# Optimization experiments

Measured on AMD Instinct MI355X. Metric: run time of the kernel, lower is better.

Reference implementation:

```python
import jax, jax.numpy as jnp
import numpy as np

N, E, F_IN, H, L = 100000, 1600000, 256, 128, 4
ALPHA, THETA, EPS = 0.1, 0.5, 1e-5


def setup_inputs() -> dict:
    key = jax.random.key(0)
    ks = jax.random.split(key, 6)
    x = jax.random.normal(ks[0], (N, F_IN), dtype=jnp.float32)
    edge_index = jax.random.randint(ks[1], (2, E), 0, N, dtype=jnp.int32)
    lin0_w = jax.random.normal(ks[2], (F_IN, H), dtype=jnp.float32) / np.sqrt(F_IN)
    lin0_b = jnp.zeros((H,), dtype=jnp.float32)
    conv_w = jax.random.normal(ks[3], (L, H, H), dtype=jnp.float32) / np.sqrt(H)
    bn_gamma = jnp.ones((L - 1, H), dtype=jnp.float32)
    bn_beta = jnp.zeros((L - 1, H), dtype=jnp.float32)
    return {"x": x, "edge_index": edge_index, "lin0_w": lin0_w, "lin0_b": lin0_b,
            "conv_w": conv_w, "bn_gamma": bn_gamma, "bn_beta": bn_beta}


def reference(x, edge_index, lin0_w, lin0_b, conv_w, bn_gamma, bn_beta):
    n = x.shape[0]
    loops = jnp.arange(n, dtype=edge_index.dtype)
    row = jnp.concatenate([edge_index[0], loops])  # source
    col = jnp.concatenate([edge_index[1], loops])  # target
    # GCN symmetric normalization with self-loops: D^{-1/2}(A+I)D^{-1/2}
    deg = jax.ops.segment_sum(jnp.ones_like(col, dtype=x.dtype), col, num_segments=n)
    dinv = jnp.where(deg > 0, jax.lax.rsqrt(deg), 0.0)
    norm = (dinv[row] * dinv[col])[:, None]  # [E+N, 1]

    def prop(h):  # sparse aggregation: out[c] += norm * h[r]
        return jax.ops.segment_sum(h[row] * norm, col, num_segments=n)

    # GCNConv input layer
    z = prop(x @ lin0_w) + lin0_b
    x0 = z
    for i in range(L):
        h = prop(z)
        beta = float(np.log(THETA / (i + 1) + 1.0))
        s = (1.0 - ALPHA) * h + ALPHA * x0          # identity mapping to initial features
        z = (1.0 - beta) * s + beta * (s @ conv_w[i])  # shared_weights GCN2Conv
        if i < L - 1:
            mu = jnp.mean(z, axis=0)
            var = jnp.mean((z - mu) ** 2, axis=0)
            z = (z - mu) * jax.lax.rsqrt(var + EPS) * bn_gamma[i] + bn_beta[i]
            z = jax.nn.relu(z)
    return z
```

## Files before the change

### kernel.cpp

```cpp
#include <hip/hip_runtime.h>
#include <hip/hip_bf16.h>
#include <math.h>

#define H 128
#define EPS_BN 1e-5f
#define RSTATS 16

typedef __attribute__((ext_vector_type(8))) short short8;
typedef __attribute__((ext_vector_type(4))) float f32x4;

__device__ __forceinline__ float bf2f(ushort u){
  union { float f; uint v; } x; x.v = ((uint)u) << 16; return x.f;
}
__device__ __forceinline__ ushort f2bf(float f){
  union { float f; uint v; } x; x.f = f;
  uint v = x.v;
  uint r = v + 0x7fff + ((v >> 16) & 1);
  return (ushort)(r >> 16);
}

__device__ __forceinline__ void acc8(float* a, uint4 v, float wt){
  a[0] += wt*bf2f((ushort)(v.x & 0xffff)); a[1] += wt*bf2f((ushort)(v.x >> 16));
  a[2] += wt*bf2f((ushort)(v.y & 0xffff)); a[3] += wt*bf2f((ushort)(v.y >> 16));
  a[4] += wt*bf2f((ushort)(v.z & 0xffff)); a[5] += wt*bf2f((ushort)(v.z >> 16));
  a[6] += wt*bf2f((ushort)(v.w & 0xffff)); a[7] += wt*bf2f((ushort)(v.w >> 16));
}


__global__ void k_count(const int* __restrict__ col, int E, int* __restrict__ cnt){
  int i = blockIdx.x*blockDim.x + threadIdx.x;
  if (i < E) atomicAdd(&cnt[col[i]], 1);
}

__global__ void k_dinv(const int* __restrict__ cnt, float* __restrict__ dinv, int n){
  int i = blockIdx.x*blockDim.x + threadIdx.x;
  if (i < n) dinv[i] = rsqrtf((float)cnt[i] + 1.0f);
}

__global__ void k_scan1(const int* __restrict__ cnt, int* __restrict__ off,
                        int* __restrict__ bsum, int n){
  __shared__ int s[1024];
  int t = threadIdx.x;
  int i = blockIdx.x*1024 + t;
  int v = (i < n) ? cnt[i] : 0;
  s[t] = v; __syncthreads();
  for (int d = 1; d < 1024; d <<= 1){
    int x = (t >= d) ? s[t-d] : 0;
    __syncthreads();
    s[t] += x;
    __syncthreads();
  }
  if (i < n) off[i] = s[t] - v;
  if (t == 1023) bsum[blockIdx.x] = s[1023];
}

__global__ void k_scan2(int* bsum, int nb){
  int l = threadIdx.x;
  int carry = 0;
  for (int b0 = 0; b0 < nb; b0 += 64){
    int i = b0 + l;
    int orig = (i < nb) ? bsum[i] : 0;
    int v = orig;
    #pragma unroll
    for (int d = 1; d < 64; d <<= 1){
      int x = __shfl_up(v, d);
      if (l >= d) v += x;
    }
    if (i < nb) bsum[i] = carry + v - orig;
    carry += __shfl(v, 63);
  }
}

__global__ void k_scan3(int* __restrict__ off, int* __restrict__ cursor,
                        const int* __restrict__ bsum, int n, int Etot){
  int i = blockIdx.x*blockDim.x + threadIdx.x;
  if (i < n){ int o = off[i] + bsum[i >> 10]; off[i] = o; cursor[i] = o; }
  if (i == 0) off[n] = Etot;
}

__global__ void k_fill(const int* __restrict__ row, const int* __restrict__ col, int E,
                       const float* __restrict__ dinv, int* __restrict__ cursor,
                       uint2* __restrict__ edge){
  int i = blockIdx.x*blockDim.x + threadIdx.x;
  if (i < E){
    int c = col[i], r = row[i];
    int p = atomicAdd(&cursor[c], 1);
    edge[p] = make_uint2((uint)r, __float_as_uint(dinv[r]*dinv[c]));
  }
}


__global__ void k_prepw(const float* __restrict__ lin0_w, const float* __restrict__ conv_w,
                        ushort* __restrict__ lin0T, ushort* __restrict__ WpT,
                        float b0, float b1, float b2, float b3){
  int i = blockIdx.x*blockDim.x + threadIdx.x;
  if (i < 128*256){
    int nn = i >> 8, k = i & 255;
    lin0T[i] = f2bf(lin0_w[k*128 + nn]);
  } else if (i < 128*256 + 4*128*128){
    int j = i - 128*256;
    int ll = j >> 14, rc = j & 16383;
    int nn = rc >> 7, k = rc & 127;
    float beta = (ll==0)?b0:(ll==1)?b1:(ll==2)?b2:b3;
    float v = beta * conv_w[ll*16384 + k*128 + nn];
    if (k == nn) v += 1.0f - beta;
    WpT[j] = f2bf(v);
  }
}


__global__ __launch_bounds__(256) void k_prop0(
    const ushort* __restrict__ h, const int* __restrict__ off,
    const uint2* __restrict__ edge, const float* __restrict__ dinv,
    const float* __restrict__ bias,
    ushort* __restrict__ x0, int n){
  int g = blockIdx.x*blockDim.x + threadIdx.x;
  int node = g >> 6;
  if (node >= n) return;
  int l = g & 63, lr = l & 15, q = l >> 4;
  int e0 = off[node], e1 = off[node+1];
  float a[8];
  #pragma unroll
  for (int j = 0; j < 8; ++j) a[j] = 0.f;
  int e = e0 + q;
  for (; e + 12 < e1; e += 16){
    uint2 edA = edge[e],   edB = edge[e+4];
    uint2 edC = edge[e+8], edD = edge[e+12];
    uint4 vA = *(const uint4*)(h + (size_t)edA.x*H + lr*8);
    uint4 vB = *(const uint4*)(h + (size_t)edB.x*H + lr*8);
    uint4 vC = *(const uint4*)(h + (size_t)edC.x*H + lr*8);
    uint4 vD = *(const uint4*)(h + (size_t)edD.x*H + lr*8);
    acc8(a, vA, __uint_as_float(edA.y));
    acc8(a, vB, __uint_as_float(edB.y));
    acc8(a, vC, __uint_as_float(edC.y));
    acc8(a, vD, __uint_as_float(edD.y));
  }
  for (; e < e1; e += 4){
    uint2 ed = edge[e];
    uint4 v = *(const uint4*)(h + (size_t)ed.x*H + lr*8);
    acc8(a, v, __uint_as_float(ed.y));
  }
  if (q == 0){
    float wc = dinv[node]; wc *= wc;
    uint4 v = *(const uint4*)(h + (size_t)node*H + lr*8);
    acc8(a, v, wc);
  }
  #pragma unroll
  for (int j = 0; j < 8; ++j){
    a[j] += __shfl(a[j], l ^ 16);
    a[j] += __shfl(a[j], l ^ 32);
  }
  if (q == 0){
    float4 b0 = *(const float4*)(bias + lr*8);
    float4 b1 = *(const float4*)(bias + lr*8 + 4);
    uint4 pk;
    pk.x = (uint)f2bf(a[0]+b0.x) | ((uint)f2bf(a[1]+b0.y) << 16);
    pk.y = (uint)f2bf(a[2]+b0.z) | ((uint)f2bf(a[3]+b0.w) << 16);
    pk.z = (uint)f2bf(a[4]+b1.x) | ((uint)f2bf(a[5]+b1.y) << 16);
    pk.w = (uint)f2bf(a[6]+b1.z) | ((uint)f2bf(a[7]+b1.w) << 16);
    *(uint4*)(x0 + (size_t)node*H + lr*8) = pk;
  }
}


template<bool STATS, bool OUTF32>
__global__ __launch_bounds__(256) void k_layer(
    const ushort* __restrict__ zin, const ushort* __restrict__ x0,
    const int* __restrict__ off, const uint2* __restrict__ edge,
    const float* __restrict__ dinv, const ushort* __restrict__ BT,
    void* __restrict__ zout, float* __restrict__ stats, int n)
{
  __shared__ ushort Sm[32*128];
  int t = threadIdx.x;
  int w = t >> 6, l = t & 63;
  int lr = l & 15, q = l >> 4;
  int base = blockIdx.x * 32;

  for (int nd = 0; nd < 8; ++nd){
    int node = base + w*8 + nd;
    float a[8];
    #pragma unroll
    for (int j = 0; j < 8; ++j) a[j] = 0.f;
    if (node < n){
      int e0 = off[node], e1 = off[node+1];
      int e = e0 + q;
      for (; e + 12 < e1; e += 16){
        uint2 edA = edge[e],   edB = edge[e+4];
        uint2 edC = edge[e+8], edD = edge[e+12];
        uint4 vA = *(const uint4*)(zin + (size_t)edA.x*H + lr*8);
        uint4 vB = *(const uint4*)(zin + (size_t)edB.x*H + lr*8);
        uint4 vC = *(const uint4*)(zin + (size_t)edC.x*H + lr*8);
        uint4 vD = *(const uint4*)(zin + (size_t)edD.x*H + lr*8);
        acc8(a, vA, __uint_as_float(edA.y));
        acc8(a, vB, __uint_as_float(edB.y));
        acc8(a, vC, __uint_as_float(edC.y));
        acc8(a, vD, __uint_as_float(edD.y));
      }
      for (; e < e1; e += 4){
        uint2 ed = edge[e];
        uint4 v = *(const uint4*)(zin + (size_t)ed.x*H + lr*8);
        acc8(a, v, __uint_as_float(ed.y));
      }
      if (q == 0){
        float wc = dinv[node]; wc *= wc;
        uint4 v = *(const uint4*)(zin + (size_t)node*H + lr*8);
        acc8(a, v, wc);
      }
    }
    #pragma unroll
    for (int j = 0; j < 8; ++j){
      a[j] += __shfl(a[j], l ^ 16);
      a[j] += __shfl(a[j], l ^ 32);
    }
    if (q == 0){
      int row = w*8 + nd;
      uint4 pk = make_uint4(0u,0u,0u,0u);
      if (node < n){
        uint4 xv = *(const uint4*)(x0 + (size_t)node*H + lr*8);
        float s0 = 0.9f*a[0] + 0.1f*bf2f((ushort)(xv.x & 0xffff));
        float s1 = 0.9f*a[1] + 0.1f*bf2f((ushort)(xv.x >> 16));
        float s2 = 0.9f*a[2] + 0.1f*bf2f((ushort)(xv.y & 0xffff));
        float s3 = 0.9f*a[3] + 0.1f*bf2f((ushort)(xv.y >> 16));
        float s4 = 0.9f*a[4] + 0.1f*bf2f((ushort)(xv.z & 0xffff));
        float s5 = 0.9f*a[5] + 0.1f*bf2f((ushort)(xv.z >> 16));
        float s6 = 0.9f*a[6] + 0.1f*bf2f((ushort)(xv.w & 0xffff));
        float s7 = 0.9f*a[7] + 0.1f*bf2f((ushort)(xv.w >> 16));
        pk.x = (uint)f2bf(s0) | ((uint)f2bf(s1) << 16);
        pk.y = (uint)f2bf(s2) | ((uint)f2bf(s3) << 16);
        pk.z = (uint)f2bf(s4) | ((uint)f2bf(s5) << 16);
        pk.w = (uint)f2bf(s6) | ((uint)f2bf(s7) << 16);
      }
      *(uint4*)(&Sm[row*128 + ((lr ^ (row & 15))*8)]) = pk;
    }
  }

  short8 bfr[2][4];
  #pragma unroll
  for (int c = 0; c < 2; ++c)
    #pragma unroll
    for (int ks = 0; ks < 4; ++ks)
      bfr[c][ks] = *(const short8*)(BT + (size_t)(w*32 + c*16 + lr)*H + ks*32 + q*8);

  __syncthreads();

  f32x4 acc[2][2];
  #pragma unroll
  for (int rt = 0; rt < 2; ++rt){
    acc[rt][0] = (f32x4){0.f,0.f,0.f,0.f};
    acc[rt][1] = (f32x4){0.f,0.f,0.f,0.f};
  }
  #pragma unroll
  for (int rt = 0; rt < 2; ++rt){
    int row = rt*16 + lr;
    #pragma unroll
    for (int ks = 0; ks < 4; ++ks){
      short8 af = *(const short8*)(&Sm[row*128 + (((ks*4 + q) ^ (row & 15))*8)]);
      acc[rt][0] = __builtin_amdgcn_mfma_f32_16x16x32_bf16(af, bfr[0][ks], acc[rt][0], 0,0,0);
      acc[rt][1] = __builtin_amdgcn_mfma_f32_16x16x32_bf16(af, bfr[1][ks], acc[rt][1], 0,0,0);
    }
  }

  #pragma unroll
  for (int rt = 0; rt < 2; ++rt){
    #pragma unroll
    for (int c = 0; c < 2; ++c){
      #pragma unroll
      for (int j = 0; j < 4; ++j){
        int row = base + rt*16 + q*4 + j;
        float v = acc[rt][c][j];
        if (OUTF32){
          if (row < n)
            ((float*)zout)[(size_t)row*H + w*32 + c*16 + lr] = v;
        } else {
          float other = __shfl(v, l ^ 1);
          if (!(lr & 1) && row < n){
            uint pk = (uint)f2bf(v) | ((uint)f2bf(other) << 16);
            ((uint*)zout)[(size_t)row*64 + w*16 + c*8 + (lr >> 1)] = pk;
          }
        }
      }
    }
  }
  if (STATS){
    #pragma unroll
    for (int c = 0; c < 2; ++c){
      float sv = 0.f, sq = 0.f;
      #pragma unroll
      for (int rt = 0; rt < 2; ++rt)
        #pragma unroll
        for (int j = 0; j < 4; ++j){
          float v = acc[rt][c][j];
          sv += v; sq += v*v;
        }
      sv += __shfl(sv, l ^ 16); sv += __shfl(sv, l ^ 32);
      sq += __shfl(sq, l ^ 16); sq += __shfl(sq, l ^ 32);
      if (q == 0){
        float* st = stats + (size_t)(blockIdx.x & (RSTATS-1))*256;
        atomicAdd(&st[w*32 + c*16 + lr], sv);
        atomicAdd(&st[128 + w*32 + c*16 + lr], sq);
      }
    }
  }
}


__global__ void k_bnfinal(const float* __restrict__ stats, const float* __restrict__ gamma,
                          const float* __restrict__ beta, float* __restrict__ scsh,
                          float inv_n){
  int f = threadIdx.x;
  float s = 0.f, s2 = 0.f;
  for (int r = 0; r < RSTATS; ++r){
    s  += stats[r*256 + f];
    s2 += stats[r*256 + 128 + f];
  }
  float mu  = s * inv_n;
  float var = s2 * inv_n - mu*mu;
  float sc  = rsqrtf(var + EPS_BN) * gamma[f];
  scsh[f]       = sc;
  scsh[128 + f] = beta[f] - mu*sc;
}


__global__ __launch_bounds__(256) void k_bnapply(
    uint4* __restrict__ z, const float* __restrict__ scsh, int n16){
  int i = blockIdx.x*blockDim.x + threadIdx.x;
  if (i >= n16) return;
  int f8 = (i & 15) * 8;
  uint4 v = z[i];
  uint r[4];
  #pragma unroll
  for (int p = 0; p < 4; ++p){
    uint  u  = (&v.x)[p];
    float z0 = bf2f((ushort)(u & 0xffff));
    float z1 = bf2f((ushort)(u >> 16));
    float y0 = fmaxf(fmaf(z0, scsh[f8 + p*2],     scsh[128 + f8 + p*2]),     0.f);
    float y1 = fmaxf(fmaf(z1, scsh[f8 + p*2 + 1], scsh[128 + f8 + p*2 + 1]), 0.f);
    r[p] = (uint)f2bf(y0) | ((uint)f2bf(y1) << 16);
  }
  z[i] = make_uint4(r[0], r[1], r[2], r[3]);
}


__global__ __launch_bounds__(256) void k_gemm0(
    const float* __restrict__ Af, const ushort* __restrict__ BT,
    ushort* __restrict__ Cb, int n){
  const int K = 256;
  __shared__ ushort As[64*32];
  __shared__ ushort Bs[128*32];
  int t = threadIdx.x;
  int br = blockIdx.x * 64;
  int w = t >> 6, l = t & 63;
  int lr = l & 15, lk = l >> 4;
  int swz = (lr >> 1) & 3;

  f32x4 acc[8];
  #pragma unroll
  for (int i = 0; i < 8; ++i) acc[i] = (f32x4){0.f,0.f,0.f,0.f};

  int sar = t >> 2;
  int sab = t & 3;
  int sa_off = sar*32 + ((sab ^ ((sar>>1)&3))*8);

  for (int k0 = 0; k0 < K; k0 += 32){
    int grow = br + sar;
    float4 v0 = make_float4(0.f,0.f,0.f,0.f), v1 = v0;
    if (grow < n){
      v0 = *(const float4*)(Af + (size_t)grow*K + k0 + sab*8);
      v1 = *(const float4*)(Af + (size_t)grow*K + k0 + sab*8 + 4);
    }
    ushort tmp[8] = {f2bf(v0.x),f2bf(v0.y),f2bf(v0.z),f2bf(v0.w),
                     f2bf(v1.x),f2bf(v1.y),f2bf(v1.z),f2bf(v1.w)};
    *(uint4*)(&As[sa_off]) = *(const uint4*)tmp;
    #pragma unroll
    for (int i = 0; i < 2; ++i){
      int qq = t + i*256;
      int nrow = qq >> 2, bb = qq & 3;
      uint4 v = *(const uint4*)(BT + (size_t)nrow*K + k0 + bb*8);
      *(uint4*)(&Bs[nrow*32 + ((bb ^ ((nrow>>1)&3))*8)]) = v;
    }
    __syncthreads();
    short8 af = *(const short8*)(&As[(w*16+lr)*32 + ((lk ^ swz)*8)]);
    #pragma unroll
    for (int tn = 0; tn < 8; ++tn){
      short8 bfv = *(const short8*)(&Bs[(tn*16+lr)*32 + ((lk ^ swz)*8)]);
      acc[tn] = __builtin_amdgcn_mfma_f32_16x16x32_bf16(af, bfv, acc[tn], 0, 0, 0);
    }
    __syncthreads();
  }
  int orow = br + w*16 + lk*4;
  #pragma unroll
  for (int tn = 0; tn < 8; ++tn){
    #pragma unroll
    for (int j = 0; j < 4; ++j){
      float mine  = acc[tn][j];
      float other = __shfl(mine, l ^ 1);
      if (!(l & 1) && (orow + j) < n){
        uint pk = (uint)f2bf(mine) | ((uint)f2bf(other) << 16);
        ((uint*)Cb)[(size_t)(orow+j)*64 + tn*8 + (lr >> 1)] = pk;
      }
    }
  }
}


extern "C" void kernel_launch(void* const* d_in, const int* in_sizes, int n_in,
                              void* d_out, int out_size, void* d_ws, size_t ws_size,
                              hipStream_t stream){
  const float* x        = (const float*)d_in[0];
  const int*   ei       = (const int*)  d_in[1];
  const float* lin0_w   = (const float*)d_in[2];
  const float* lin0_b   = (const float*)d_in[3];
  const float* conv_w   = (const float*)d_in[4];
  const float* bn_gamma = (const float*)d_in[5];
  const float* bn_beta  = (const float*)d_in[6];
  float* out = (float*)d_out;

  int N = in_sizes[0] / 256;
  int E = in_sizes[1] / 2;
  const int* row = ei;
  const int* col = ei + E;

  char* ws = (char*)d_ws;
  size_t p = 0;
  auto alloc = [&](size_t bytes)->char*{
    char* r = ws + p; p = (p + bytes + 255) & ~(size_t)255; return r;
  };
  int*    cnt    = (int*)   alloc((size_t)N*4);
  int*    off    = (int*)   alloc((size_t)(N+1)*4);
  int*    cursor = (int*)   alloc((size_t)N*4);
  float*  dinv   = (float*) alloc((size_t)N*4);
  int*    bsum   = (int*)   alloc(512*4);
  uint2*  edge   = (uint2*) alloc((size_t)E*8);
  ushort* zb     = (ushort*)alloc((size_t)N*H*2);
  ushort* sb     = (ushort*)alloc((size_t)N*H*2);
  ushort* x0b    = (ushort*)alloc((size_t)N*H*2);
  ushort* lin0T  = (ushort*)alloc(128*256*2);
  ushort* WpT    = (ushort*)alloc(4*128*128*2);
  float*  stats  = (float*) alloc(RSTATS*256*4);
  float*  scsh   = (float*) alloc(2*128*4);

  float betas[4];
  for (int i = 0; i < 4; ++i) betas[i] = logf(0.5f/(float)(i+1) + 1.0f);
  float inv_n = 1.0f/(float)N;

  hipMemsetAsync(cnt, 0, (size_t)N*4, stream);
  k_count<<<(E+255)/256, 256, 0, stream>>>(col, E, cnt);
  k_dinv <<<(N+255)/256, 256, 0, stream>>>(cnt, dinv, N);
  int nb = (N + 1023)/1024;
  k_scan1<<<nb, 1024, 0, stream>>>(cnt, off, bsum, N);
  k_scan2<<<1, 64, 0, stream>>>(bsum, nb);
  k_scan3<<<(N+255)/256, 256, 0, stream>>>(off, cursor, bsum, N, E);
  k_fill <<<(E+255)/256, 256, 0, stream>>>(row, col, E, dinv, cursor, edge);

  k_prepw<<<(128*256 + 4*128*128 + 255)/256, 256, 0, stream>>>(
      lin0_w, conv_w, lin0T, WpT, betas[0], betas[1], betas[2], betas[3]);

  int gemm_blocks = (N + 63)/64;
  int lay_blocks  = (N + 31)/32;
  int prop_blocks = ((N*64) + 255)/256;
  int bn_blocks   = ((N*16) + 255)/256;

  k_gemm0<<<gemm_blocks, 256, 0, stream>>>(x, lin0T, sb, N);
  k_prop0<<<prop_blocks, 256, 0, stream>>>(sb, off, edge, dinv, lin0_b, x0b, N);

  hipMemsetAsync(stats, 0, RSTATS*256*4, stream);
  k_layer<true,false><<<lay_blocks, 256, 0, stream>>>(
      x0b, x0b, off, edge, dinv, WpT + 0*128*128, sb, stats, N);
  k_bnfinal<<<1, 128, 0, stream>>>(stats, bn_gamma + 0*H, bn_beta + 0*H, scsh, inv_n);
  k_bnapply<<<bn_blocks, 256, 0, stream>>>((uint4*)sb, scsh, N*16);

  hipMemsetAsync(stats, 0, RSTATS*256*4, stream);
  k_layer<true,false><<<lay_blocks, 256, 0, stream>>>(
      sb, x0b, off, edge, dinv, WpT + 1*128*128, zb, stats, N);
  k_bnfinal<<<1, 128, 0, stream>>>(stats, bn_gamma + 1*H, bn_beta + 1*H, scsh, inv_n);
  k_bnapply<<<bn_blocks, 256, 0, stream>>>((uint4*)zb, scsh, N*16);

  hipMemsetAsync(stats, 0, RSTATS*256*4, stream);
  k_layer<true,false><<<lay_blocks, 256, 0, stream>>>(
      zb, x0b, off, edge, dinv, WpT + 2*128*128, sb, stats, N);
  k_bnfinal<<<1, 128, 0, stream>>>(stats, bn_gamma + 2*H, bn_beta + 2*H, scsh, inv_n);
  k_bnapply<<<bn_blocks, 256, 0, stream>>>((uint4*)sb, scsh, N*16);

  k_layer<false,true><<<lay_blocks, 256, 0, stream>>>(
      sb, x0b, off, edge, dinv, WpT + 3*128*128, out, nullptr, N);
}
```

Before: 697.3 us.

## Assign one 16-lane group per node in sparse gathers instead of a wavefront

Changes the work mapping of the sparse aggregation in both k_prop0 and k_layer so each 16-lane quarter-wave handles a whole node, walking all of its edges serially. Previously a full 64-lane wavefront split a node's edges four ways and then reduced them with cross-lane shuffles. The change removes the shuffle reduction and the idle lanes on low-degree nodes (about 16 neighbours on average), and gives each wavefront four nodes' gathers in flight. In exchange each lane runs a longer serial edge loop, and degree imbalance between the four nodes sharing a wavefront can cause divergence.

```diff
diff --git a/kernel.cpp b/kernel.cpp
--- a/kernel.cpp
+++ b/kernel.cpp
@@ -109,57 +109,54 @@
 }
 
 
+__device__ __forceinline__ void gather_node(
+    float* a, const ushort* __restrict__ zin, const uint2* __restrict__ edge,
+    const float* __restrict__ dinv, int node, int e0, int e1, int lr){
+  float wc = dinv[node]; wc *= wc;
+  uint4 vs = *(const uint4*)(zin + (size_t)node*H + lr*8);
+  int e = e0;
+  for (; e + 3 < e1; e += 4){
+    uint2 er0 = edge[e],   er1 = edge[e+1];
+    uint2 er2 = edge[e+2], er3 = edge[e+3];
+    uint4 v0 = *(const uint4*)(zin + (size_t)er0.x*H + lr*8);
+    uint4 v1 = *(const uint4*)(zin + (size_t)er1.x*H + lr*8);
+    uint4 v2 = *(const uint4*)(zin + (size_t)er2.x*H + lr*8);
+    uint4 v3 = *(const uint4*)(zin + (size_t)er3.x*H + lr*8);
+    acc8(a, v0, __uint_as_float(er0.y));
+    acc8(a, v1, __uint_as_float(er1.y));
+    acc8(a, v2, __uint_as_float(er2.y));
+    acc8(a, v3, __uint_as_float(er3.y));
+  }
+  for (; e < e1; ++e){
+    uint2 er = edge[e];
+    uint4 v = *(const uint4*)(zin + (size_t)er.x*H + lr*8);
+    acc8(a, v, __uint_as_float(er.y));
+  }
+  acc8(a, vs, wc);
+}
+
+
 __global__ __launch_bounds__(256) void k_prop0(
     const ushort* __restrict__ h, const int* __restrict__ off,
     const uint2* __restrict__ edge, const float* __restrict__ dinv,
     const float* __restrict__ bias,
     ushort* __restrict__ x0, int n){
-  int g = blockIdx.x*blockDim.x + threadIdx.x;
-  int node = g >> 6;
-  if (node >= n) return;
-  int l = g & 63, lr = l & 15, q = l >> 4;
-  int e0 = off[node], e1 = off[node+1];
+  int gq = (blockIdx.x*blockDim.x + threadIdx.x) >> 4;
+  if (gq >= n) return;
+  int lr = threadIdx.x & 15;
+  int e0 = off[gq], e1 = off[gq+1];
   float a[8];
   #pragma unroll
   for (int j = 0; j < 8; ++j) a[j] = 0.f;
-  int e = e0 + q;
-  for (; e + 12 < e1; e += 16){
-    uint2 edA = edge[e],   edB = edge[e+4];
-    uint2 edC = edge[e+8], edD = edge[e+12];
-    uint4 vA = *(const uint4*)(h + (size_t)edA.x*H + lr*8);
-    uint4 vB = *(const uint4*)(h + (size_t)edB.x*H + lr*8);
-    uint4 vC = *(const uint4*)(h + (size_t)edC.x*H + lr*8);
-    uint4 vD = *(const uint4*)(h + (size_t)edD.x*H + lr*8);
-    acc8(a, vA, __uint_as_float(edA.y));
-    acc8(a, vB, __uint_as_float(edB.y));
-    acc8(a, vC, __uint_as_float(edC.y));
-    acc8(a, vD, __uint_as_float(edD.y));
-  }
-  for (; e < e1; e += 4){
-    uint2 ed = edge[e];
-    uint4 v = *(const uint4*)(h + (size_t)ed.x*H + lr*8);
-    acc8(a, v, __uint_as_float(ed.y));
-  }
-  if (q == 0){
-    float wc = dinv[node]; wc *= wc;
-    uint4 v = *(const uint4*)(h + (size_t)node*H + lr*8);
-    acc8(a, v, wc);
-  }
-  #pragma unroll
-  for (int j = 0; j < 8; ++j){
-    a[j] += __shfl(a[j], l ^ 16);
-    a[j] += __shfl(a[j], l ^ 32);
-  }
-  if (q == 0){
-    float4 b0 = *(const float4*)(bias + lr*8);
-    float4 b1 = *(const float4*)(bias + lr*8 + 4);
-    uint4 pk;
-    pk.x = (uint)f2bf(a[0]+b0.x) | ((uint)f2bf(a[1]+b0.y) << 16);
-    pk.y = (uint)f2bf(a[2]+b0.z) | ((uint)f2bf(a[3]+b0.w) << 16);
-    pk.z = (uint)f2bf(a[4]+b1.x) | ((uint)f2bf(a[5]+b1.y) << 16);
-    pk.w = (uint)f2bf(a[6]+b1.z) | ((uint)f2bf(a[7]+b1.w) << 16);
-    *(uint4*)(x0 + (size_t)node*H + lr*8) = pk;
-  }
+  gather_node(a, h, edge, dinv, gq, e0, e1, lr);
+  float4 b0 = *(const float4*)(bias + lr*8);
+  float4 b1 = *(const float4*)(bias + lr*8 + 4);
+  uint4 pk;
+  pk.x = (uint)f2bf(a[0]+b0.x) | ((uint)f2bf(a[1]+b0.y) << 16);
+  pk.y = (uint)f2bf(a[2]+b0.z) | ((uint)f2bf(a[3]+b0.w) << 16);
+  pk.z = (uint)f2bf(a[4]+b1.x) | ((uint)f2bf(a[5]+b1.y) << 16);
+  pk.w = (uint)f2bf(a[6]+b1.z) | ((uint)f2bf(a[7]+b1.w) << 16);
+  *(uint4*)(x0 + (size_t)gq*H + lr*8) = pk;
 }
 
 
@@ -176,62 +173,32 @@
   int lr = l & 15, q = l >> 4;
   int base = blockIdx.x * 32;
 
-  for (int nd = 0; nd < 8; ++nd){
-    int node = base + w*8 + nd;
+  #pragma unroll
+  for (int g2 = 0; g2 < 2; ++g2){
+    int row  = w*8 + g2*4 + q;
+    int node = base + row;
     float a[8];
     #pragma unroll
     for (int j = 0; j < 8; ++j) a[j] = 0.f;
+    uint4 pk = make_uint4(0u,0u,0u,0u);
     if (node < n){
       int e0 = off[node], e1 = off[node+1];
-      int e = e0 + q;
-      for (; e + 12 < e1; e += 16){
-        uint2 edA = edge[e],   edB = edge[e+4];
-        uint2 edC = edge[e+8], edD = edge[e+12];
-        uint4 vA = *(const uint4*)(zin + (size_t)edA.x*H + lr*8);
-        uint4 vB = *(const uint4*)(zin + (size_t)edB.x*H + lr*8);
-        uint4 vC = *(const uint4*)(zin + (size_t)edC.x*H + lr*8);
-        uint4 vD = *(const uint4*)(zin + (size_t)edD.x*H + lr*8);
-        acc8(a, vA, __uint_as_float(edA.y));
-        acc8(a, vB, __uint_as_float(edB.y));
-        acc8(a, vC, __uint_as_float(edC.y));
-        acc8(a, vD, __uint_as_float(edD.y));
-      }
-      for (; e < e1; e += 4){
-        uint2 ed = edge[e];
-        uint4 v = *(const uint4*)(zin + (size_t)ed.x*H + lr*8);
-        acc8(a, v, __uint_as_float(ed.y));
-      }
-      if (q == 0){
-        float wc = dinv[node]; wc *= wc;
-        uint4 v = *(const uint4*)(zin + (size_t)node*H + lr*8);
-        acc8(a, v, wc);
-      }
-    }
-    #pragma unroll
-    for (int j = 0; j < 8; ++j){
-      a[j] += __shfl(a[j], l ^ 16);
-      a[j] += __shfl(a[j], l ^ 32);
-    }
-    if (q == 0){
-      int row = w*8 + nd;
-      uint4 pk = make_uint4(0u,0u,0u,0u);
-      if (node < n){
-        uint4 xv = *(const uint4*)(x0 + (size_t)node*H + lr*8);
-        float s0 = 0.9f*a[0] + 0.1f*bf2f((ushort)(xv.x & 0xffff));
-        float s1 = 0.9f*a[1] + 0.1f*bf2f((ushort)(xv.x >> 16));
-        float s2 = 0.9f*a[2] + 0.1f*bf2f((ushort)(xv.y & 0xffff));
-        float s3 = 0.9f*a[3] + 0.1f*bf2f((ushort)(xv.y >> 16));
-        float s4 = 0.9f*a[4] + 0.1f*bf2f((ushort)(xv.z & 0xffff));
-        float s5 = 0.9f*a[5] + 0.1f*bf2f((ushort)(xv.z >> 16));
-        float s6 = 0.9f*a[6] + 0.1f*bf2f((ushort)(xv.w & 0xffff));
-        float s7 = 0.9f*a[7] + 0.1f*bf2f((ushort)(xv.w >> 16));
-        pk.x = (uint)f2bf(s0) | ((uint)f2bf(s1) << 16);
-        pk.y = (uint)f2bf(s2) | ((uint)f2bf(s3) << 16);
-        pk.z = (uint)f2bf(s4) | ((uint)f2bf(s5) << 16);
-        pk.w = (uint)f2bf(s6) | ((uint)f2bf(s7) << 16);
-      }
-      *(uint4*)(&Sm[row*128 + ((lr ^ (row & 15))*8)]) = pk;
-    }
+      gather_node(a, zin, edge, dinv, node, e0, e1, lr);
+      uint4 xv = *(const uint4*)(x0 + (size_t)node*H + lr*8);
+      float s0 = 0.9f*a[0] + 0.1f*bf2f((ushort)(xv.x & 0xffff));
+      float s1 = 0.9f*a[1] + 0.1f*bf2f((ushort)(xv.x >> 16));
+      float s2 = 0.9f*a[2] + 0.1f*bf2f((ushort)(xv.y & 0xffff));
+      float s3 = 0.9f*a[3] + 0.1f*bf2f((ushort)(xv.y >> 16));
+      float s4 = 0.9f*a[4] + 0.1f*bf2f((ushort)(xv.z & 0xffff));
+      float s5 = 0.9f*a[5] + 0.1f*bf2f((ushort)(xv.z >> 16));
+      float s6 = 0.9f*a[6] + 0.1f*bf2f((ushort)(xv.w & 0xffff));
+      float s7 = 0.9f*a[7] + 0.1f*bf2f((ushort)(xv.w >> 16));
+      pk.x = (uint)f2bf(s0) | ((uint)f2bf(s1) << 16);
+      pk.y = (uint)f2bf(s2) | ((uint)f2bf(s3) << 16);
+      pk.z = (uint)f2bf(s4) | ((uint)f2bf(s5) << 16);
+      pk.w = (uint)f2bf(s6) | ((uint)f2bf(s7) << 16);
+    }
+    *(uint4*)(&Sm[row*128 + ((lr ^ (row & 15))*8)]) = pk;
   }
 
   short8 bfr[2][4];
@@ -457,7 +424,7 @@
 
   int gemm_blocks = (N + 63)/64;
   int lay_blocks  = (N + 31)/32;
-  int prop_blocks = ((N*64) + 255)/256;
+  int prop_blocks = (N + 15)/16;
   int bn_blocks   = ((N*16) + 255)/256;
 
   k_gemm0<<<gemm_blocks, 256, 0, stream>>>(x, lin0T, sb, N);
```

Result: faster. 613.1 us (-12.1%).
